# Optimization experiments

Measured on AMD Instinct MI355X. Metric: run time of the kernel, lower is better.

The kernel has to match this reference:

```python
import jax, jax.numpy as jnp
import numpy as np

BITS = 4
SPLIT_BITS = 4  # `ratio` arg plays the role of split_bits in the torch Function


def _chunk_quant(src, bits):
    """src: [n_chunks, chunk_elems...]; quantize each chunk with its own min/max."""
    reduce_axes = tuple(range(1, src.ndim))
    mn = src.min(axis=reduce_axes, keepdims=True)
    mx = src.max(axis=reduce_axes, keepdims=True)
    levels = jnp.asarray(2 ** bits - 1, src.dtype)
    step = (mx - mn) / levels
    safe_step = jnp.where(step == 0, jnp.ones_like(step), step)
    # torch: round((s-min)/step) - 2^(b-1); then (+2^(b-1))*step + min  ==  round(...)*step + min
    q = jnp.round((src - mn) / safe_step) * safe_step + mn
    # if min == max the chunk is passed through unchanged
    return jnp.where(mn == mx, src, q)


def setup_inputs() -> dict:
    key = jax.random.key(0)
    x = jax.random.normal(key, (16, 2048, 2048), dtype=jnp.float32)
    return {"x": x}


def reference(x) -> jnp.ndarray:
    shape = x.shape
    flat = x.reshape(-1)
    n_chunks = 2 ** SPLIT_BITS  # 16; flat.size divisible by 16 by construction
    order = jnp.argsort(flat)            # ascending sort permutation
    src = flat[order].reshape(n_chunks, -1)
    q = _chunk_quant(src, BITS).reshape(-1)
    # scatter quantized values back to original positions: out[order[i]] = q[i]
    inv = jnp.argsort(order)
    out = q[inv]
    return out.reshape(shape)
```

## Files before the change

kernel.cpp:

```cpp
#include <hip/hip_runtime.h>
#include <math.h>

#define L1B 4096
#define L2B 512
#define L3B 2048
#define SLOTS 32
#define H1_BLOCKS 512
#define H2_BLOCKS 256
#define H2_WORDS (SLOTS * L2B / 2)

__device__ unsigned int g_part1[H1_BLOCKS * L1B];
__device__ unsigned int g_part2[H2_BLOCKS * H2_WORDS];
__device__ unsigned int g_hist1[L1B];
__device__ unsigned int g_hist2[SLOTS * L2B];
__device__ unsigned int g_hist3[SLOTS * L3B];
__device__ unsigned char g_sid1[L1B];
__device__ unsigned char g_sid2[SLOTS * L2B];

__device__ unsigned int g_bin1[32], g_res1[32];
__device__ int          g_slot1[32];
__device__ unsigned int g_bin2[32], g_res2[32];
__device__ int          g_slot2[32];
__device__ unsigned int g_bin3[32], g_res3[32];
__device__ float        g_mn[16], g_mx[16];
__device__ unsigned int g_tkey[16];

__device__ __forceinline__ unsigned int f2key(float f) {
    unsigned int b = __float_as_uint(f);
    return (b & 0x80000000u) ? ~b : (b | 0x80000000u);
}
__device__ __forceinline__ float key2f(unsigned int k) {
    unsigned int b = (k & 0x80000000u) ? (k & 0x7FFFFFFFu) : ~k;
    return __uint_as_float(b);
}

__global__ void zero_scratch() {
    int i = blockIdx.x * blockDim.x + threadIdx.x;
    int stride = gridDim.x * blockDim.x;
    for (int j = i; j < SLOTS * L3B; j += stride) g_hist3[j] = 0u;
    unsigned int* s1 = (unsigned int*)g_sid1;
    for (int j = i; j < L1B / 4; j += stride) s1[j] = 0u;
    unsigned int* s2 = (unsigned int*)g_sid2;
    for (int j = i; j < SLOTS * L2B / 4; j += stride) s2[j] = 0u;
}

__global__ void hist1_kernel(const float4* __restrict__ x, int n4) {
    __shared__ unsigned int h[2 * L1B];
    for (int j = threadIdx.x; j < 2 * L1B; j += blockDim.x) h[j] = 0u;
    __syncthreads();
    unsigned int* hp = &h[((threadIdx.x >> 6) & 1) * L1B];
    int stride = gridDim.x * blockDim.x;
    for (int i = blockIdx.x * blockDim.x + threadIdx.x; i < n4; i += stride) {
        float4 v = x[i];
        atomicAdd(&hp[f2key(v.x) >> 20], 1u);
        atomicAdd(&hp[f2key(v.y) >> 20], 1u);
        atomicAdd(&hp[f2key(v.z) >> 20], 1u);
        atomicAdd(&hp[f2key(v.w) >> 20], 1u);
    }
    __syncthreads();
    for (int j = threadIdx.x; j < L1B; j += blockDim.x)
        g_part1[blockIdx.x * L1B + j] = h[j] + h[L1B + j];
}

__global__ void reduce1_kernel() {
    int j = blockIdx.x * blockDim.x + threadIdx.x;
    if (j >= L1B) return;
    unsigned int s = 0;
    for (int b = 0; b < H1_BLOCKS; ++b) s += g_part1[b * L1B + j];
    g_hist1[j] = s;
}

__device__ void wave_select(const unsigned int* __restrict__ hist, int nbins,
                            unsigned int r, unsigned int* out_bin, unsigned int* out_res) {
    int lane = threadIdx.x & 63;
    unsigned int base = 0;
    for (int k = 0; k < nbins; k += 64) {
        unsigned int v = hist[k + lane];
        unsigned int incl = v;
#pragma unroll
        for (int off = 1; off < 64; off <<= 1) {
            unsigned int t = (unsigned int)__shfl_up((int)incl, off, 64);
            if (lane >= off) incl += t;
        }
        unsigned int total = (unsigned int)__shfl((int)incl, 63, 64);
        if (r < base + total) {
            unsigned long long m = __ballot(base + incl > r);
            int fl = __ffsll((long long)m) - 1;
            unsigned int incl_fl = (unsigned int)__shfl((int)incl, fl, 64);
            unsigned int v_fl = (unsigned int)__shfl((int)v, fl, 64);
            if (lane == 0) {
                *out_bin = (unsigned int)(k + fl);
                *out_res = r - (base + incl_fl - v_fl);
            }
            return;
        }
        base += total;
    }
}

__global__ void select1_kernel(unsigned int n) {
    int i = blockIdx.x;
    unsigned int M = n >> 4;
    unsigned int c = (unsigned int)(i >> 1);
    unsigned int r = (i & 1) ? ((c + 1) * M - 1u) : (c * M);
    wave_select(g_hist1, L1B, r, &g_bin1[i], &g_res1[i]);
}

__global__ void assign1_kernel() {
    if (threadIdx.x != 0 || blockIdx.x != 0) return;
    int nslot = 0;
    for (int i = 0; i < 32; ++i) {
        unsigned int b = g_bin1[i];
        if (g_sid1[b] == 0) g_sid1[b] = (unsigned char)(++nslot);
        g_slot1[i] = g_sid1[b] - 1;
    }
}

__global__ void hist2_kernel(const float4* __restrict__ x, int n4) {
    __shared__ unsigned int h2[H2_WORDS];
    __shared__ unsigned char sid1[L1B];
    for (int j = threadIdx.x; j < H2_WORDS; j += blockDim.x) h2[j] = 0u;
    unsigned int* s1w = (unsigned int*)sid1;
    for (int j = threadIdx.x; j < L1B / 4; j += blockDim.x) s1w[j] = ((const unsigned int*)g_sid1)[j];
    __syncthreads();
    int stride = gridDim.x * blockDim.x;
    for (int i = blockIdx.x * blockDim.x + threadIdx.x; i < n4; i += stride) {
        float4 v = x[i];
        float vv[4] = {v.x, v.y, v.z, v.w};
#pragma unroll
        for (int k = 0; k < 4; ++k) {
            unsigned int key = f2key(vv[k]);
            unsigned int s = sid1[key >> 20];
            if (s) {
                unsigned int c = ((s - 1) << 9) | ((key >> 11) & (L2B - 1));
                atomicAdd(&h2[c >> 1], 1u << ((c & 1) << 4));
            }
        }
    }
    __syncthreads();
    for (int j = threadIdx.x; j < H2_WORDS; j += blockDim.x)
        g_part2[blockIdx.x * H2_WORDS + j] = h2[j];
}

__global__ void reduce2_kernel() {
    int w = blockIdx.x * blockDim.x + threadIdx.x;
    if (w >= H2_WORDS) return;
    unsigned int lo = 0, hi = 0;
    for (int b = 0; b < H2_BLOCKS; ++b) {
        unsigned int u = g_part2[b * H2_WORDS + w];
        lo += u & 0xFFFFu;
        hi += u >> 16;
    }
    g_hist2[2 * w] = lo;
    g_hist2[2 * w + 1] = hi;
}

__global__ void select2_kernel() {
    int i = blockIdx.x;
    int s = g_slot1[i];
    wave_select(g_hist2 + s * L2B, L2B, g_res1[i], &g_bin2[i], &g_res2[i]);
}

__global__ void assign2_kernel() {
    if (threadIdx.x != 0 || blockIdx.x != 0) return;
    int nslot = 0;
    for (int i = 0; i < 32; ++i) {
        int p = g_slot1[i] * L2B + (int)g_bin2[i];
        if (g_sid2[p] == 0) g_sid2[p] = (unsigned char)(++nslot);
        g_slot2[i] = g_sid2[p] - 1;
    }
}

__global__ void hist3_kernel(const float4* __restrict__ x, int n4) {
    __shared__ unsigned char sid1[L1B];
    __shared__ unsigned char sid2[SLOTS * L2B];
    unsigned int* s1w = (unsigned int*)sid1;
    for (int j = threadIdx.x; j < L1B / 4; j += blockDim.x) s1w[j] = ((const unsigned int*)g_sid1)[j];
    unsigned int* s2w = (unsigned int*)sid2;
    for (int j = threadIdx.x; j < SLOTS * L2B / 4; j += blockDim.x) s2w[j] = ((const unsigned int*)g_sid2)[j];
    __syncthreads();
    int stride = gridDim.x * blockDim.x;
    for (int i = blockIdx.x * blockDim.x + threadIdx.x; i < n4; i += stride) {
        float4 v = x[i];
        float vv[4] = {v.x, v.y, v.z, v.w};
#pragma unroll
        for (int k = 0; k < 4; ++k) {
            unsigned int key = f2key(vv[k]);
            unsigned int s = sid1[key >> 20];
            if (s) {
                unsigned int s2 = sid2[((s - 1) << 9) | ((key >> 11) & (L2B - 1))];
                if (s2) atomicAdd(&g_hist3[((s2 - 1) << 11) | (key & (L3B - 1))], 1u);
            }
        }
    }
}

__global__ void select3_kernel() {
    int i = blockIdx.x;
    int s2 = g_slot2[i];
    wave_select(g_hist3 + s2 * L3B, L3B, g_res2[i], &g_bin3[i], &g_res3[i]);
}

__global__ void finalize_kernel() {
    int c = threadIdx.x;
    if (c < 16) {
        unsigned int klo = (g_bin1[2 * c] << 20) | (g_bin2[2 * c] << 11) | g_bin3[2 * c];
        unsigned int khi = (g_bin1[2 * c + 1] << 20) | (g_bin2[2 * c + 1] << 11) | g_bin3[2 * c + 1];
        g_mn[c] = key2f(klo);
        g_mx[c] = key2f(khi);
        g_tkey[c] = (c == 0) ? 0u : klo;
    }
}

__global__ void quant_kernel(const float4* __restrict__ x, float4* __restrict__ out, int n4) {
    __shared__ float s_mn[16], s_mx[16];
    __shared__ unsigned int s_t[16];
    if (threadIdx.x < 16) {
        s_mn[threadIdx.x] = g_mn[threadIdx.x];
        s_mx[threadIdx.x] = g_mx[threadIdx.x];
        s_t[threadIdx.x]  = g_tkey[threadIdx.x];
    }
    __syncthreads();
    int stride = gridDim.x * blockDim.x;
    for (int i = blockIdx.x * blockDim.x + threadIdx.x; i < n4; i += stride) {
        float4 v = x[i];
        float r[4] = {v.x, v.y, v.z, v.w};
#pragma unroll
        for (int k = 0; k < 4; ++k) {
            float xv = r[k];
            unsigned int key = f2key(xv);
            int c = (key >= s_t[8]) ? 8 : 0;
            if (key >= s_t[c + 4]) c += 4;
            if (key >= s_t[c + 2]) c += 2;
            if (key >= s_t[c + 1]) c += 1;
            float mn = s_mn[c], mx = s_mx[c];
            float outv;
            if (mn == mx) {
                outv = xv;
            } else {
                float st = (mx - mn) / 15.0f;
                if (st == 0.0f) st = 1.0f;
                float q = rintf((xv - mn) / st);
                outv = __fadd_rn(__fmul_rn(q, st), mn);
            }
            r[k] = outv;
        }
        out[i] = make_float4(r[0], r[1], r[2], r[3]);
    }
}

extern "C" void kernel_launch(void* const* d_in, const int* in_sizes, int n_in,
                              void* d_out, int out_size, void* d_ws, size_t ws_size,
                              hipStream_t stream) {
    const float* x = (const float*)d_in[0];
    float* out = (float*)d_out;
    int n  = in_sizes[0];
    int n4 = n / 4;

    zero_scratch<<<128, 256, 0, stream>>>();
    hist1_kernel<<<H1_BLOCKS, 512, 0, stream>>>((const float4*)x, n4);
    reduce1_kernel<<<16, 256, 0, stream>>>();
    select1_kernel<<<32, 64, 0, stream>>>((unsigned int)n);
    assign1_kernel<<<1, 64, 0, stream>>>();
    hist2_kernel<<<H2_BLOCKS, 512, 0, stream>>>((const float4*)x, n4);
    reduce2_kernel<<<32, 256, 0, stream>>>();
    select2_kernel<<<32, 64, 0, stream>>>();
    assign2_kernel<<<1, 64, 0, stream>>>();
    hist3_kernel<<<2048, 256, 0, stream>>>((const float4*)x, n4);
    select3_kernel<<<32, 64, 0, stream>>>();
    finalize_kernel<<<1, 64, 0, stream>>>();
    quant_kernel<<<4096, 256, 0, stream>>>((const float4*)x, (float4*)out, n4);
}
```

Before: 742.2 us.

## Compact candidate keys after first pass; histogram later radix levels over compacted keys

After the first-level histogram selects the candidate top bins, a compaction kernel writes the keys of elements falling in those bins to a global buffer. The second- and third-level histograms then scan only this compacted key list instead of rereading the full 256MB input twice. Reductions are split into two stages for more parallelism, select and assign kernels are merged into single-block kernels, and the hist1 sub-histogram split now interleaves by thread parity with padding. The cost is an extra write of the candidate keys plus a ballot/shared-atomic compaction with periodic flushes, and it relies on a fixed-size global buffer sized for the maximum element count.

```diff
diff --git a/kernel.cpp b/kernel.cpp
--- a/kernel.cpp
+++ b/kernel.cpp
@@ -5,13 +5,20 @@
 #define L2B 512
 #define L3B 2048
 #define SLOTS 32
+#define NMAX 67108864
 #define H1_BLOCKS 512
-#define H2_BLOCKS 256
-#define H2_WORDS (SLOTS * L2B / 2)
-
+#define H2C_BLOCKS 256
+#define H2W (SLOTS * L2B / 2)
+#define H1PAD (L1B + 8)
+#define CCAP 8192
+
+__device__ __align__(16) unsigned int g_keys[NMAX];
+__device__ unsigned int g_nkeys;
 __device__ unsigned int g_part1[H1_BLOCKS * L1B];
-__device__ unsigned int g_part2[H2_BLOCKS * H2_WORDS];
+__device__ unsigned int g_r1tmp[16 * L1B];
 __device__ unsigned int g_hist1[L1B];
+__device__ unsigned int g_part2[H2C_BLOCKS * H2W];
+__device__ unsigned int g_r2lo[8 * H2W], g_r2hi[8 * H2W];
 __device__ unsigned int g_hist2[SLOTS * L2B];
 __device__ unsigned int g_hist3[SLOTS * L3B];
 __device__ unsigned char g_sid1[L1B];
@@ -21,7 +28,6 @@
 __device__ int          g_slot1[32];
 __device__ unsigned int g_bin2[32], g_res2[32];
 __device__ int          g_slot2[32];
-__device__ unsigned int g_bin3[32], g_res3[32];
 __device__ float        g_mn[16], g_mx[16];
 __device__ unsigned int g_tkey[16];
 
@@ -42,13 +48,14 @@
     for (int j = i; j < L1B / 4; j += stride) s1[j] = 0u;
     unsigned int* s2 = (unsigned int*)g_sid2;
     for (int j = i; j < SLOTS * L2B / 4; j += stride) s2[j] = 0u;
+    if (i == 0) g_nkeys = 0u;
 }
 
 __global__ void hist1_kernel(const float4* __restrict__ x, int n4) {
-    __shared__ unsigned int h[2 * L1B];
-    for (int j = threadIdx.x; j < 2 * L1B; j += blockDim.x) h[j] = 0u;
-    __syncthreads();
-    unsigned int* hp = &h[((threadIdx.x >> 6) & 1) * L1B];
+    __shared__ unsigned int h[2 * H1PAD];
+    for (int j = threadIdx.x; j < 2 * H1PAD; j += blockDim.x) h[j] = 0u;
+    __syncthreads();
+    unsigned int* hp = &h[(threadIdx.x & 1) * H1PAD];
     int stride = gridDim.x * blockDim.x;
     for (int i = blockIdx.x * blockDim.x + threadIdx.x; i < n4; i += stride) {
         float4 v = x[i];
@@ -59,19 +66,26 @@
     }
     __syncthreads();
     for (int j = threadIdx.x; j < L1B; j += blockDim.x)
-        g_part1[blockIdx.x * L1B + j] = h[j] + h[L1B + j];
-}
-
-__global__ void reduce1_kernel() {
+        g_part1[blockIdx.x * L1B + j] = h[j] + h[H1PAD + j];
+}
+
+__global__ void reduce1_s1() {
+    int t = blockIdx.x * blockDim.x + threadIdx.x;
+    int j = t & (L1B - 1);
+    int g = t >> 12;
+    unsigned int s = 0;
+    for (int b = g * 32; b < g * 32 + 32; ++b) s += g_part1[b * L1B + j];
+    g_r1tmp[g * L1B + j] = s;
+}
+__global__ void reduce1_s2() {
     int j = blockIdx.x * blockDim.x + threadIdx.x;
-    if (j >= L1B) return;
     unsigned int s = 0;
-    for (int b = 0; b < H1_BLOCKS; ++b) s += g_part1[b * L1B + j];
+    for (int g = 0; g < 16; ++g) s += g_r1tmp[g * L1B + j];
     g_hist1[j] = s;
 }
 
-__device__ void wave_select(const unsigned int* __restrict__ hist, int nbins,
-                            unsigned int r, unsigned int* out_bin, unsigned int* out_res) {
+__device__ void wave_select(const unsigned int* hist, int nbins, unsigned int r,
+                            unsigned int* out_bin, unsigned int* out_res) {
     int lane = threadIdx.x & 63;
     unsigned int base = 0;
     for (int k = 0; k < nbins; k += 64) {
@@ -99,79 +113,167 @@
 }
 
 __global__ void select1_kernel(unsigned int n) {
-    int i = blockIdx.x;
+    __shared__ unsigned int s_hist[L1B];
+    __shared__ unsigned int s_bin[32], s_res[32];
+    for (int j = threadIdx.x; j < L1B; j += blockDim.x) s_hist[j] = g_hist1[j];
+    __syncthreads();
     unsigned int M = n >> 4;
-    unsigned int c = (unsigned int)(i >> 1);
-    unsigned int r = (i & 1) ? ((c + 1) * M - 1u) : (c * M);
-    wave_select(g_hist1, L1B, r, &g_bin1[i], &g_res1[i]);
-}
-
-__global__ void assign1_kernel() {
-    if (threadIdx.x != 0 || blockIdx.x != 0) return;
-    int nslot = 0;
-    for (int i = 0; i < 32; ++i) {
-        unsigned int b = g_bin1[i];
-        if (g_sid1[b] == 0) g_sid1[b] = (unsigned char)(++nslot);
-        g_slot1[i] = g_sid1[b] - 1;
-    }
-}
-
-__global__ void hist2_kernel(const float4* __restrict__ x, int n4) {
-    __shared__ unsigned int h2[H2_WORDS];
-    __shared__ unsigned char sid1[L1B];
-    for (int j = threadIdx.x; j < H2_WORDS; j += blockDim.x) h2[j] = 0u;
-    unsigned int* s1w = (unsigned int*)sid1;
-    for (int j = threadIdx.x; j < L1B / 4; j += blockDim.x) s1w[j] = ((const unsigned int*)g_sid1)[j];
-    __syncthreads();
-    int stride = gridDim.x * blockDim.x;
-    for (int i = blockIdx.x * blockDim.x + threadIdx.x; i < n4; i += stride) {
-        float4 v = x[i];
+    int w = threadIdx.x >> 6;
+    for (int i = w; i < 32; i += 16) {
+        unsigned int c = (unsigned int)(i >> 1);
+        unsigned int r = (i & 1) ? ((c + 1) * M - 1u) : (c * M);
+        wave_select(s_hist, L1B, r, &s_bin[i], &s_res[i]);
+    }
+    __syncthreads();
+    if (threadIdx.x == 0) {
+        unsigned int ubin[32]; int ns = 0;
+        for (int i = 0; i < 32; ++i) {
+            unsigned int b = s_bin[i];
+            int sl = -1;
+            for (int k = 0; k < ns; ++k) if (ubin[k] == b) { sl = k; break; }
+            if (sl < 0) { sl = ns; ubin[ns++] = b; g_sid1[b] = (unsigned char)(sl + 1); }
+            g_bin1[i] = b; g_res1[i] = s_res[i]; g_slot1[i] = sl;
+        }
+    }
+}
+
+__global__ void __launch_bounds__(512) compact_kernel(const float4* __restrict__ x, int n4) {
+    __shared__ unsigned int buf[CCAP];
+    __shared__ unsigned char sid[L1B];
+    __shared__ unsigned int s_cnt, s_base;
+    unsigned int* sw = (unsigned int*)sid;
+    for (int j = threadIdx.x; j < L1B / 4; j += blockDim.x) sw[j] = ((const unsigned int*)g_sid1)[j];
+    if (threadIdx.x == 0) s_cnt = 0u;
+    __syncthreads();
+
+    int lane = threadIdx.x & 63;
+    unsigned long long lanemask = (1ull << lane) - 1ull;
+    int NT = gridDim.x * blockDim.x;
+    int kIters = (n4 + NT - 1) / NT;
+    int i0 = blockIdx.x * blockDim.x + threadIdx.x;
+
+    for (int it = 0; it < kIters; ++it) {
+        int i = i0 + it * NT;
+        float4 v;
+        bool inb = (i < n4);
+        if (inb) v = x[i];
         float vv[4] = {v.x, v.y, v.z, v.w};
 #pragma unroll
         for (int k = 0; k < 4; ++k) {
-            unsigned int key = f2key(vv[k]);
-            unsigned int s = sid1[key >> 20];
-            if (s) {
-                unsigned int c = ((s - 1) << 9) | ((key >> 11) & (L2B - 1));
-                atomicAdd(&h2[c >> 1], 1u << ((c & 1) << 4));
+            unsigned int key = inb ? f2key(vv[k]) : 0u;
+            bool act = inb && (sid[key >> 20] != 0);
+            unsigned long long m = __ballot(act);
+            if (m) {
+                int leader = __ffsll((long long)m) - 1;
+                unsigned int pos = 0;
+                if (lane == leader) pos = atomicAdd(&s_cnt, (unsigned int)__popcll(m));
+                pos = (unsigned int)__shfl((int)pos, leader, 64);
+                if (act) buf[pos + (unsigned int)__popcll(m & lanemask)] = key;
             }
         }
-    }
-    __syncthreads();
-    for (int j = threadIdx.x; j < H2_WORDS; j += blockDim.x)
-        g_part2[blockIdx.x * H2_WORDS + j] = h2[j];
-}
-
-__global__ void reduce2_kernel() {
-    int w = blockIdx.x * blockDim.x + threadIdx.x;
-    if (w >= H2_WORDS) return;
+        if ((it & 1) == 1) {
+            __syncthreads();
+            unsigned int c = s_cnt;
+            if (c > CCAP - 4096) {
+                if (threadIdx.x == 0) s_base = atomicAdd(&g_nkeys, c);
+                __syncthreads();
+                for (unsigned int j = threadIdx.x; j < c; j += blockDim.x)
+                    g_keys[s_base + j] = buf[j];
+                __syncthreads();
+                if (threadIdx.x == 0) s_cnt = 0u;
+                __syncthreads();
+            }
+        }
+    }
+    __syncthreads();
+    unsigned int c = s_cnt;
+    if (c) {
+        if (threadIdx.x == 0) s_base = atomicAdd(&g_nkeys, c);
+        __syncthreads();
+        for (unsigned int j = threadIdx.x; j < c; j += blockDim.x)
+            g_keys[s_base + j] = buf[j];
+    }
+}
+
+__global__ void hist2c_kernel() {
+    __shared__ unsigned int h2[H2W];
+    __shared__ unsigned char sid[L1B];
+    for (int j = threadIdx.x; j < H2W; j += blockDim.x) h2[j] = 0u;
+    unsigned int* sw = (unsigned int*)sid;
+    for (int j = threadIdx.x; j < L1B / 4; j += blockDim.x) sw[j] = ((const unsigned int*)g_sid1)[j];
+    __syncthreads();
+    unsigned int nk = g_nkeys;
+    unsigned int nk4 = nk >> 2;
+    int stride = gridDim.x * blockDim.x;
+    const uint4* k4 = (const uint4*)g_keys;
+    for (unsigned int i = blockIdx.x * blockDim.x + threadIdx.x; i < nk4; i += stride) {
+        uint4 kk = k4[i];
+        unsigned int ks[4] = {kk.x, kk.y, kk.z, kk.w};
+#pragma unroll
+        for (int k = 0; k < 4; ++k) {
+            unsigned int key = ks[k];
+            unsigned int s = sid[key >> 20];
+            unsigned int c = ((s - 1) << 9) | ((key >> 11) & (L2B - 1));
+            atomicAdd(&h2[c >> 1], 1u << ((c & 1) << 4));
+        }
+    }
+    {
+        unsigned int t = (unsigned int)(blockIdx.x * blockDim.x + threadIdx.x);
+        unsigned int base = nk & ~3u;
+        if (t < (nk & 3u)) {
+            unsigned int key = g_keys[base + t];
+            unsigned int s = sid[key >> 20];
+            unsigned int c = ((s - 1) << 9) | ((key >> 11) & (L2B - 1));
+            atomicAdd(&h2[c >> 1], 1u << ((c & 1) << 4));
+        }
+    }
+    __syncthreads();
+    for (int j = threadIdx.x; j < H2W; j += blockDim.x)
+        g_part2[blockIdx.x * H2W + j] = h2[j];
+}
+
+__global__ void reduce2_s1() {
+    int t = blockIdx.x * blockDim.x + threadIdx.x;
+    int w = t & (H2W - 1);
+    int g = t >> 13;
     unsigned int lo = 0, hi = 0;
-    for (int b = 0; b < H2_BLOCKS; ++b) {
-        unsigned int u = g_part2[b * H2_WORDS + w];
-        lo += u & 0xFFFFu;
-        hi += u >> 16;
-    }
-    g_hist2[2 * w] = lo;
-    g_hist2[2 * w + 1] = hi;
+    for (int b = g * 32; b < g * 32 + 32; ++b) {
+        unsigned int u = g_part2[b * H2W + w];
+        lo += u & 0xFFFFu; hi += u >> 16;
+    }
+    g_r2lo[g * H2W + w] = lo;
+    g_r2hi[g * H2W + w] = hi;
+}
+__global__ void reduce2_s2() {
+    int c = blockIdx.x * blockDim.x + threadIdx.x;
+    int w = c >> 1, half = c & 1;
+    unsigned int s = 0;
+    if (half) { for (int g = 0; g < 8; ++g) s += g_r2hi[g * H2W + w]; }
+    else      { for (int g = 0; g < 8; ++g) s += g_r2lo[g * H2W + w]; }
+    g_hist2[c] = s;
 }
 
 __global__ void select2_kernel() {
-    int i = blockIdx.x;
-    int s = g_slot1[i];
-    wave_select(g_hist2 + s * L2B, L2B, g_res1[i], &g_bin2[i], &g_res2[i]);
-}
-
-__global__ void assign2_kernel() {
-    if (threadIdx.x != 0 || blockIdx.x != 0) return;
-    int nslot = 0;
-    for (int i = 0; i < 32; ++i) {
-        int p = g_slot1[i] * L2B + (int)g_bin2[i];
-        if (g_sid2[p] == 0) g_sid2[p] = (unsigned char)(++nslot);
-        g_slot2[i] = g_sid2[p] - 1;
-    }
-}
-
-__global__ void hist3_kernel(const float4* __restrict__ x, int n4) {
+    __shared__ unsigned int s_bin[32], s_res[32];
+    int w = threadIdx.x >> 6;
+    for (int i = w; i < 32; i += 16) {
+        int s = g_slot1[i];
+        wave_select(g_hist2 + s * L2B, L2B, g_res1[i], &s_bin[i], &s_res[i]);
+    }
+    __syncthreads();
+    if (threadIdx.x == 0) {
+        int upos[32]; int ns = 0;
+        for (int i = 0; i < 32; ++i) {
+            int p = g_slot1[i] * L2B + (int)s_bin[i];
+            int sl = -1;
+            for (int k = 0; k < ns; ++k) if (upos[k] == p) { sl = k; break; }
+            if (sl < 0) { sl = ns; upos[ns++] = p; g_sid2[p] = (unsigned char)(sl + 1); }
+            g_bin2[i] = s_bin[i]; g_res2[i] = s_res[i]; g_slot2[i] = sl;
+        }
+    }
+}
+
+__global__ void hist3c_kernel() {
     __shared__ unsigned char sid1[L1B];
     __shared__ unsigned char sid2[SLOTS * L2B];
     unsigned int* s1w = (unsigned int*)sid1;
@@ -179,33 +281,45 @@
     unsigned int* s2w = (unsigned int*)sid2;
     for (int j = threadIdx.x; j < SLOTS * L2B / 4; j += blockDim.x) s2w[j] = ((const unsigned int*)g_sid2)[j];
     __syncthreads();
-    int stride = gridDim.x * blockDim.x;
-    for (int i = blockIdx.x * blockDim.x + threadIdx.x; i < n4; i += stride) {
-        float4 v = x[i];
-        float vv[4] = {v.x, v.y, v.z, v.w};
+    unsigned int nk = g_nkeys;
+    unsigned int nk4 = nk >> 2;
+    int stride = gridDim.x * blockDim.x;
+    const uint4* k4 = (const uint4*)g_keys;
+    for (unsigned int i = blockIdx.x * blockDim.x + threadIdx.x; i < nk4; i += stride) {
+        uint4 kk = k4[i];
+        unsigned int ks[4] = {kk.x, kk.y, kk.z, kk.w};
 #pragma unroll
         for (int k = 0; k < 4; ++k) {
-            unsigned int key = f2key(vv[k]);
-            unsigned int s = sid1[key >> 20];
-            if (s) {
-                unsigned int s2 = sid2[((s - 1) << 9) | ((key >> 11) & (L2B - 1))];
-                if (s2) atomicAdd(&g_hist3[((s2 - 1) << 11) | (key & (L3B - 1))], 1u);
-            }
+            unsigned int key = ks[k];
+            unsigned int s1 = sid1[key >> 20];
+            unsigned int s2 = sid2[((s1 - 1) << 9) | ((key >> 11) & (L2B - 1))];
+            if (s2) atomicAdd(&g_hist3[((s2 - 1) << 11) | (key & (L3B - 1))], 1u);
+        }
+    }
+    {
+        unsigned int t = (unsigned int)(blockIdx.x * blockDim.x + threadIdx.x);
+        unsigned int base = nk & ~3u;
+        if (t < (nk & 3u)) {
+            unsigned int key = g_keys[base + t];
+            unsigned int s1 = sid1[key >> 20];
+            unsigned int s2 = sid2[((s1 - 1) << 9) | ((key >> 11) & (L2B - 1))];
+            if (s2) atomicAdd(&g_hist3[((s2 - 1) << 11) | (key & (L3B - 1))], 1u);
         }
     }
 }
 
 __global__ void select3_kernel() {
-    int i = blockIdx.x;
-    int s2 = g_slot2[i];
-    wave_select(g_hist3 + s2 * L3B, L3B, g_res2[i], &g_bin3[i], &g_res3[i]);
-}
-
-__global__ void finalize_kernel() {
-    int c = threadIdx.x;
-    if (c < 16) {
-        unsigned int klo = (g_bin1[2 * c] << 20) | (g_bin2[2 * c] << 11) | g_bin3[2 * c];
-        unsigned int khi = (g_bin1[2 * c + 1] << 20) | (g_bin2[2 * c + 1] << 11) | g_bin3[2 * c + 1];
+    __shared__ unsigned int s_bin[32], s_res[32];
+    int w = threadIdx.x >> 6;
+    for (int i = w; i < 32; i += 16) {
+        int s2 = g_slot2[i];
+        wave_select(g_hist3 + s2 * L3B, L3B, g_res2[i], &s_bin[i], &s_res[i]);
+    }
+    __syncthreads();
+    if (threadIdx.x < 16) {
+        int c = threadIdx.x;
+        unsigned int klo = (g_bin1[2 * c] << 20) | (g_bin2[2 * c] << 11) | s_bin[2 * c];
+        unsigned int khi = (g_bin1[2 * c + 1] << 20) | (g_bin2[2 * c + 1] << 11) | s_bin[2 * c + 1];
         g_mn[c] = key2f(klo);
         g_mx[c] = key2f(khi);
         g_tkey[c] = (c == 0) ? 0u : klo;
@@ -259,15 +373,15 @@
 
     zero_scratch<<<128, 256, 0, stream>>>();
     hist1_kernel<<<H1_BLOCKS, 512, 0, stream>>>((const float4*)x, n4);
-    reduce1_kernel<<<16, 256, 0, stream>>>();
-    select1_kernel<<<32, 64, 0, stream>>>((unsigned int)n);
-    assign1_kernel<<<1, 64, 0, stream>>>();
-    hist2_kernel<<<H2_BLOCKS, 512, 0, stream>>>((const float4*)x, n4);
-    reduce2_kernel<<<32, 256, 0, stream>>>();
-    select2_kernel<<<32, 64, 0, stream>>>();
-    assign2_kernel<<<1, 64, 0, stream>>>();
-    hist3_kernel<<<2048, 256, 0, stream>>>((const float4*)x, n4);
-    select3_kernel<<<32, 64, 0, stream>>>();
-    finalize_kernel<<<1, 64, 0, stream>>>();
+    reduce1_s1<<<256, 256, 0, stream>>>();
+    reduce1_s2<<<16, 256, 0, stream>>>();
+    select1_kernel<<<1, 1024, 0, stream>>>((unsigned int)n);
+    compact_kernel<<<512, 512, 0, stream>>>((const float4*)x, n4);
+    hist2c_kernel<<<H2C_BLOCKS, 256, 0, stream>>>();
+    reduce2_s1<<<256, 256, 0, stream>>>();
+    reduce2_s2<<<64, 256, 0, stream>>>();
+    select2_kernel<<<1, 1024, 0, stream>>>();
+    hist3c_kernel<<<256, 256, 0, stream>>>();
+    select3_kernel<<<1, 1024, 0, stream>>>();
     quant_kernel<<<4096, 256, 0, stream>>>((const float4*)x, (float4*)out, n4);
 }
```

Result: slower. 802.2 us (+8.1%).
